# Optimization experiments

Hardware: AMD Instinct MI355X
Metric: run time of the kernel (lower is better)

The kernel has to match this reference:

```python
import jax, jax.numpy as jnp
import numpy as np

# Static config (matches init_kwargs)
DIM, HEADS = 192, 6
PL, LAT, LON = 8, 96, 180
WP, WL, WW = 2, 6, 12          # window size (pressure, lat, lon)
SP, SL, SW = 1, 3, 6           # shift size
N = WP * WL * WW               # tokens per window = 144
NPL, NLAT, NLON = PL // WP, LAT // WL, LON // WW   # 4, 16, 15
NW = NPL * NLAT                # type_of_windows = 64 (lat/pl-dependent bias)
HD = DIM // HEADS              # 32
L = PL * LAT * LON
BIAS_LEN = (2 * WW - 1) * WL * WL * WP * WP   # 3312
EPS = 1e-5


def _position_index():
    # Earth-specific relative position index (Pangu): absolute-position
    # dependence along pressure and latitude, relative along longitude.
    zi = np.arange(WP); zj = -np.arange(WP) * WP
    hi = np.arange(WL); hj = -np.arange(WL) * WL
    w = np.arange(WW)
    c1 = np.stack(np.meshgrid(zi, hi, w, indexing='ij')).reshape(3, -1)
    c2 = np.stack(np.meshgrid(zj, hj, w, indexing='ij')).reshape(3, -1)
    c = (c1[:, :, None] - c2[:, None, :]).transpose(1, 2, 0).copy()
    c[:, :, 2] += WW - 1
    c[:, :, 1] *= 2 * WW - 1
    c[:, :, 0] *= (2 * WW - 1) * WL * WL
    return c.sum(-1)  # (N, N) in [0, BIAS_LEN)


def _attn_mask():
    # Shifted-window mask: lon is periodic on the globe (roll only), so
    # masking is applied along pressure and latitude boundaries only.
    img = np.zeros((1, PL, LAT, LON, 1), np.float32)
    cnt = 0
    for pl in (slice(0, -WP), slice(-WP, -SP), slice(-SP, None)):
        for la in (slice(0, -WL), slice(-WL, -SL), slice(-SL, None)):
            img[:, pl, la, :, :] = cnt
            cnt += 1
    mw = img.reshape(1, NPL, WP, NLAT, WL, NLON, WW, 1)
    mw = mw.transpose(0, 5, 1, 3, 2, 4, 6, 7).reshape(NLON, NW, N)
    am = mw[:, :, None, :] - mw[:, :, :, None]
    return np.where(am != 0, -100.0, 0.0).astype(np.float32)  # (NLON, NW, N, N)


POS_IDX = jnp.asarray(_position_index())
ATTN_MASK = jnp.asarray(_attn_mask())


def layer_norm(x, g, b):
    m = x.mean(-1, keepdims=True)
    v = ((x - m) ** 2).mean(-1, keepdims=True)
    return (x - m) * jax.lax.rsqrt(v + EPS) * g + b


def setup_inputs() -> dict:
    key = jax.random.key(0)
    ks = jax.random.split(key, 10)
    s = 0.02
    return {
        'x': jax.random.normal(ks[0], (1, L, DIM), jnp.float32),
        'norm1_g': jnp.ones((DIM,), jnp.float32),
        'norm1_b': jnp.zeros((DIM,), jnp.float32),
        'qkv_w': jax.random.normal(ks[1], (DIM, 3 * DIM), jnp.float32) * s,
        'qkv_b': jnp.zeros((3 * DIM,), jnp.float32),
        'earth_bias': jax.random.normal(ks[2], (BIAS_LEN, NW, HEADS), jnp.float32) * s,
        'proj_w': jax.random.normal(ks[3], (DIM, DIM), jnp.float32) * s,
        'proj_b': jnp.zeros((DIM,), jnp.float32),
        'norm2_g': jnp.ones((DIM,), jnp.float32),
        'norm2_b': jnp.zeros((DIM,), jnp.float32),
        'fc1_w': jax.random.normal(ks[4], (DIM, 4 * DIM), jnp.float32) * s,
        'fc1_b': jnp.zeros((4 * DIM,), jnp.float32),
        'fc2_w': jax.random.normal(ks[5], (4 * DIM, DIM), jnp.float32) * s,
        'fc2_b': jnp.zeros((DIM,), jnp.float32),
    }


def reference(x, norm1_g, norm1_b, qkv_w, qkv_b, earth_bias, proj_w, proj_b,
              norm2_g, norm2_b, fc1_w, fc1_b, fc2_w, fc2_b):
    B, Ltok, C = x.shape
    shortcut = x
    h = layer_norm(x, norm1_g, norm1_b).reshape(B, PL, LAT, LON, C)
    # shifted windows (lon is periodic -> plain roll)
    h = jnp.roll(h, shift=(-SP, -SL, -SW), axis=(1, 2, 3))
    # window partition -> (B*NLON, NW, N, C); lon windows folded into batch
    xw = h.reshape(B, NPL, WP, NLAT, WL, NLON, WW, C)
    xw = xw.transpose(0, 5, 1, 3, 2, 4, 6, 7).reshape(B * NLON, NW, N, C)
    # earth-specific attention
    qkv = (xw @ qkv_w + qkv_b).reshape(B * NLON, NW, N, 3, HEADS, HD)
    qkv = qkv.transpose(3, 0, 1, 4, 2, 5)  # (3, B_, NW, H, N, HD)
    q, k, v = qkv[0], qkv[1], qkv[2]
    attn = jnp.einsum('bwhnd,bwhmd->bwhnm', q * (HD ** -0.5), k)
    bias = earth_bias[POS_IDX].reshape(N, N, NW, HEADS).transpose(2, 3, 0, 1)
    attn = attn + bias[None]                        # (B_, NW, H, N, N)
    attn = attn.reshape(B, NLON, NW, HEADS, N, N) + ATTN_MASK[None, :, :, None]
    attn = jax.nn.softmax(attn.reshape(B * NLON, NW, HEADS, N, N), axis=-1)
    out = jnp.einsum('bwhnm,bwhmd->bwhnd', attn, v)
    out = out.transpose(0, 1, 3, 2, 4).reshape(B * NLON, NW, N, C)
    out = out @ proj_w + proj_b
    # window reverse + roll back
    h = out.reshape(B, NLON, NPL, NLAT, WP, WL, WW, C)
    h = h.transpose(0, 2, 4, 3, 5, 1, 6, 7).reshape(B, PL, LAT, LON, C)
    h = jnp.roll(h, shift=(SP, SL, SW), axis=(1, 2, 3)).reshape(B, Ltok, C)
    x = shortcut + h
    # MLP block (GELU exact, as nn.GELU default)
    y = layer_norm(x, norm2_g, norm2_b)
    y = jax.nn.gelu(y @ fc1_w + fc1_b, approximate=False) @ fc2_w + fc2_b
    return x + y
```

## Files before the change

kernel.cpp:

```cpp
#include <hip/hip_runtime.h>
#include <hip/hip_bf16.h>
#include <math.h>

typedef unsigned short u16;
typedef __attribute__((ext_vector_type(8))) short short8;
typedef __attribute__((ext_vector_type(4))) short short4v;
typedef __attribute__((ext_vector_type(4))) float f32x4;

#define MFMA(a,b,c) __builtin_amdgcn_mfma_f32_16x16x32_bf16(a,b,c,0,0,0)
#define DIM 192

__device__ __forceinline__ float bf2f(u16 u){ unsigned v=((unsigned)u)<<16; float f; __builtin_memcpy(&f,&v,4); return f; }
__device__ __forceinline__ u16 f2bf(float f){ unsigned v; __builtin_memcpy(&v,&f,4); v = v + 0x7fffu + ((v>>16)&1u); return (u16)(v>>16); }

__device__ __forceinline__ void gl_lds16(const u16* g, u16* l){
  __builtin_amdgcn_global_load_lds((const __attribute__((address_space(1))) unsigned int*)g,
                                   (__attribute__((address_space(3))) unsigned int*)l, 16, 0, 0);
}

__device__ __forceinline__ int win_to_tok(int r){
  int lon = r/9216; int rem = r - lon*9216;
  int w = rem/144, n = rem - w*144;
  int ip=w>>4, il=w&15;
  int wp=n/72, t=n-wp*72, wl=t/12, ww=t-wl*12;
  int p=ip*2+wp, la=il*6+wl, lo=lon*12+ww;
  int p0=p+1;  if(p0>=8)   p0-=8;
  int la0=la+3; if(la0>=96) la0-=96;
  int lo0=lo+6; if(lo0>=180)lo0-=180;
  return (p0*96+la0)*180+lo0;
}

__global__ __launch_bounds__(256) void ln1_window_kernel(
    const float* __restrict__ x, const float* __restrict__ g, const float* __restrict__ b,
    u16* __restrict__ A)
{
  int r = blockIdx.x*4 + (threadIdx.x>>6);
  int lane = threadIdx.x & 63;
  size_t src = (size_t)win_to_tok(r)*DIM;
  float v0=x[src+lane], v1=x[src+64+lane], v2=x[src+128+lane];
  float s=v0+v1+v2;
  for(int m=32;m>=1;m>>=1) s += __shfl_xor(s,m);
  float mean = s*(1.f/192.f);
  float d0=v0-mean,d1=v1-mean,d2=v2-mean;
  float q=d0*d0+d1*d1+d2*d2;
  for(int m=32;m>=1;m>>=1) q += __shfl_xor(q,m);
  float rstd = rsqrtf(q*(1.f/192.f)+1e-5f);
  size_t o = (size_t)r*DIM;
  A[o+lane]     = f2bf(d0*rstd*g[lane]     + b[lane]);
  A[o+64+lane]  = f2bf(d1*rstd*g[64+lane]  + b[64+lane]);
  A[o+128+lane] = f2bf(d2*rstd*g[128+lane] + b[128+lane]);
}

__global__ __launch_bounds__(256) void transpose_bf16_kernel(
    const float* __restrict__ src, u16* __restrict__ dst, int K, int N)
{
  int idx = blockIdx.x*256 + threadIdx.x;
  if (idx >= K*N) return;
  int k = idx / N, n = idx - k*N;
  dst[n*K + k] = f2bf(src[idx]);
}

__global__ __launch_bounds__(256) void pf_w1_kernel(const float* __restrict__ fc1w, u16* __restrict__ W1f){
  int idx = blockIdx.x*256 + threadIdx.x;
  int e = idx & 7, g3 = idx >> 3;
  int g = g3 % 24, r3 = g3 / 24;
  int r = r3 & 31, hc = r3 >> 5;
  int k = ((g ^ (r&7))<<3) + e;
  W1f[idx] = f2bf(fc1w[(size_t)k*768 + hc*32 + r]);
}
__global__ __launch_bounds__(256) void pf_w2_kernel(const float* __restrict__ fc2w, u16* __restrict__ W2f){
  int idx = blockIdx.x*256 + threadIdx.x;
  int e = idx & 7, g3 = idx >> 3;
  int g = g3 & 3, r3 = g3 >> 2;
  int r = r3 % 192, hc = r3 / 192;
  int k = hc*32 + ((g ^ (r&3))<<3) + e;
  W2f[idx] = f2bf(fc2w[(size_t)k*192 + r]);
}

__global__ __launch_bounds__(256) void bias_expand_kernel(
    const float* __restrict__ eb, u16* __restrict__ B2)
{
  __shared__ int t1s[144], t2s[144], rgs[144];
  __shared__ float ebs[3312];
  int bid = blockIdx.x;
  int w = bid / 6;
  int tid = threadIdx.x;
  if (tid < 144) {
    int n = tid;
    int wp=n/72, t=n-wp*72, wl=t/12, ww=t-wl*12;
    t1s[n] = wp*828 + wl*23 + ww;
    t2s[n] = 1656*wp + 138*wl - ww + 11;
    int ip = w>>4, il = w&15;
    int p = ip*2+wp, la = il*6+wl;
    int rp = (p<6)?0:((p<7)?1:2);
    int rl = (la<90)?0:((la<93)?1:2);
    rgs[n] = rp*3+rl;
  }
  for (int i = tid; i < 3312; i += 256) ebs[i] = eb[(size_t)i*384 + bid];
  __syncthreads();
  size_t ob = (size_t)bid*20736;
  for (int idx = tid; idx < 20736; idx += 256) {
    int i = idx & 3, lane = (idx>>2)&63, t = idx>>8;
    int mt = t%9, nt = t/9;
    int n = nt*16 + (lane&15);
    int m = mt*16 + ((lane>>4)<<2) + i;
    float bv = ebs[t1s[n]+t2s[m]];
    bv += (rgs[n]==rgs[m]) ? 0.f : -100.f;
    B2[ob + idx] = f2bf(bv);
  }
}

#define SM_WS   0
#define SM_QS   36864
#define SM_KS   48384
#define SM_VS   59904
#define SM_PS   0
#define SMEM3   70656

__global__ __launch_bounds__(576) void attn_kernel(
    const u16* __restrict__ A,
    const u16* __restrict__ Wt,
    const float* __restrict__ qkvb,
    const u16* __restrict__ Bexp,
    u16* __restrict__ O)
{
  extern __shared__ char smem[];
  u16* Ws = (u16*)(smem + SM_WS);
  u16* qs = (u16*)(smem + SM_QS);
  u16* ks_= (u16*)(smem + SM_KS);
  u16* vs = (u16*)(smem + SM_VS);
  u16* Ps = (u16*)(smem + SM_PS);

  int bid = blockIdx.x;
  int logical = (bid & 7)*720 + (bid >> 3);
  int lon = logical % 15;
  int wh  = logical / 15;
  int h = wh % 6, w = wh / 6;
  int tid = threadIdx.x, lane = tid & 63, wv = tid >> 6;

  {
    int rr = tid % 96, chunk = tid / 96;
    int mat = rr >> 5, c = rr & 31;
    const u16* s = Wt + (size_t)(mat*192 + h*32 + c)*192 + chunk*32;
    uint4 t0 = *(const uint4*)(s);
    uint4 t1 = *(const uint4*)(s+8);
    uint4 t2 = *(const uint4*)(s+16);
    uint4 t3 = *(const uint4*)(s+24);
    u16* d = Ws + rr*192;
    int r7 = rr & 7, g0 = chunk*4;
    *(uint4*)(d + ((g0  )^r7)*8) = t0;
    *(uint4*)(d + ((g0+1)^r7)*8) = t1;
    *(uint4*)(d + ((g0+2)^r7)*8) = t2;
    *(uint4*)(d + ((g0+3)^r7)*8) = t3;
  }
  if (tid < 512) { int c = tid>>4; vs[c*168 + 144 + (tid&15)] = 0; }
  __syncthreads();

  size_t winbase = (size_t)(lon*64 + w)*144;
  int r0 = wv*16;
  int l15 = lane & 15, lg = lane >> 4;
  int sw7 = l15 & 7;

  short8 af[6];
  {
    const u16* arow = A + (winbase + r0 + l15)*DIM + 8*lg;
    #pragma unroll
    for (int k0=0;k0<6;k0++) af[k0] = *(const short8*)(arow + k0*32);
  }
  const float qscale = 0.17677669529663687f;

  #pragma unroll
  for (int mt=0; mt<2; mt++) {
    f32x4 acc = {0.f,0.f,0.f,0.f};
    const u16* wrow = Ws + (mt*16 + l15)*192;
    #pragma unroll
    for (int k0=0;k0<6;k0++) acc = MFMA(*(const short8*)(wrow + ((k0*4+lg)^sw7)*8), af[k0], acc);
    short4v pk;
    #pragma unroll
    for (int i=0;i<4;i++) pk[i] = (short)f2bf((acc[i] + qkvb[h*32 + mt*16 + 4*lg + i])*qscale);
    *(short4v*)(qs + (r0 + l15)*40 + mt*16 + 4*lg) = pk;
  }
  #pragma unroll
  for (int mt=0; mt<2; mt++) {
    f32x4 acc = {0.f,0.f,0.f,0.f};
    const u16* wrow = Ws + (32 + mt*16 + l15)*192;
    #pragma unroll
    for (int k0=0;k0<6;k0++) acc = MFMA(*(const short8*)(wrow + ((k0*4+lg)^sw7)*8), af[k0], acc);
    short4v pk;
    #pragma unroll
    for (int i=0;i<4;i++) pk[i] = (short)f2bf(acc[i] + qkvb[192 + h*32 + mt*16 + 4*lg + i]);
    *(short4v*)(ks_ + (r0 + l15)*40 + mt*16 + 4*lg) = pk;
  }
  #pragma unroll
  for (int ct=0; ct<2; ct++) {
    f32x4 acc = {0.f,0.f,0.f,0.f};
    const u16* wrow = Ws + (64 + ct*16 + l15)*192;
    #pragma unroll
    for (int k0=0;k0<6;k0++) acc = MFMA(af[k0], *(const short8*)(wrow + ((k0*4+lg)^sw7)*8), acc);
    float bias = qkvb[384 + h*32 + ct*16 + l15];
    short4v pk;
    #pragma unroll
    for (int i=0;i<4;i++) pk[i] = (short)f2bf(acc[i] + bias);
    *(short4v*)(vs + (ct*16 + l15)*168 + r0 + 4*lg) = pk;
  }
  __syncthreads();

  short8 bq = *(const short8*)(qs + (r0 + l15)*40 + 8*lg);
  f32x4 sa[9];
  #pragma unroll
  for (int mt=0; mt<9; mt++) {
    f32x4 z = {0.f,0.f,0.f,0.f};
    sa[mt] = MFMA(*(const short8*)(ks_ + (mt*16 + l15)*40 + 8*lg), bq, z);
  }
  __syncthreads();

  {
    const u16* bb = Bexp + (((size_t)wh*9 + wv)*9)*256 + lane*4;
    #pragma unroll
    for (int mt=0; mt<9; mt++) {
      short4v pk = *(const short4v*)(bb + mt*256);
      #pragma unroll
      for (int i=0;i<4;i++) sa[mt][i] += bf2f((u16)pk[i]);
    }
  }
  float rsum = 0.f;
  #pragma unroll
  for (int mt=0; mt<9; mt++)
    #pragma unroll
    for (int i=0;i<4;i++) { float e = __expf(sa[mt][i]); sa[mt][i] = e; rsum += e; }
  rsum += __shfl_xor(rsum, 16);
  rsum += __shfl_xor(rsum, 32);
  float rinv = 1.f / rsum;
  #pragma unroll
  for (int mt=0; mt<9; mt++) {
    short4v pk;
    #pragma unroll
    for (int i=0;i<4;i++) pk[i] = (short)f2bf(sa[mt][i]);
    *(short4v*)(Ps + (r0 + l15)*168 + mt*16 + 4*lg) = pk;
  }
  {
    short4v z = {0,0,0,0};
    *(short4v*)(Ps + (r0 + l15)*168 + 144 + 4*lg) = z;
  }

  #pragma unroll
  for (int ct2=0; ct2<2; ct2++) {
    f32x4 acc = {0.f,0.f,0.f,0.f};
    const u16* vr = vs + (ct2*16 + l15)*168 + 8*lg;
    const u16* pr = Ps + (r0 + l15)*168 + 8*lg;
    #pragma unroll
    for (int k0=0;k0<5;k0++) acc = MFMA(*(const short8*)(vr + 32*k0), *(const short8*)(pr + 32*k0), acc);
    short4v pk;
    #pragma unroll
    for (int i=0;i<4;i++) pk[i] = (short)f2bf(acc[i]*rinv);
    *(short4v*)(O + (winbase + r0 + l15)*DIM + h*32 + ct2*16 + 4*lg) = pk;
  }
}

#define SMEMF 74240
__global__ __launch_bounds__(512, 4) void fused_tail_kernel(
    u16* __restrict__ AT,
    const u16* __restrict__ Pw,
    const float* __restrict__ pb, const float* __restrict__ x,
    const float* __restrict__ n2g, const float* __restrict__ n2b,
    const u16* __restrict__ W1f,
    const float* __restrict__ b1,
    const u16* __restrict__ W2f,
    const float* __restrict__ b2,
    float* __restrict__ out)
{
  extern __shared__ char smem[];
  u16* Pws  = (u16*)smem;
  u16* Ys   = (u16*)smem;
  u16* W1b0 = (u16*)smem;
  u16* W1b1 = (u16*)(smem + 12288);
  u16* W2b0 = (u16*)(smem + 24576);
  u16* W2b1 = (u16*)(smem + 36864);
  u16* Hs   = (u16*)(smem + 49152);
  int* tokmap = (int*)(smem + 73728);
  int tid = threadIdx.x;
  size_t rbase = (size_t)blockIdx.x*128;
  int lane = tid&63, wv = tid>>6, r0 = wv*16;
  int l15 = lane&15, lg = lane>>4;

  #pragma unroll
  for (int j=0;j<9;j++){
    int g = j*512 + tid;
    int row = g/24, jj = g - row*24;
    uint4 t = *(const uint4*)(Pw + (size_t)row*192 + jj*8);
    *(uint4*)(Pws + row*192 + ((jj ^ (row&7))*8)) = t;
  }
  if (tid < 128) tokmap[tid] = win_to_tok((int)rbase + tid);
  __syncthreads();

  short8 af[6];
  {
    const u16* arow = AT + (rbase + r0 + l15)*DIM + 8*lg;
    #pragma unroll
    for (int k0=0;k0<6;k0++) af[k0] = *(const short8*)(arow + k0*32);
  }
  f32x4 acc[12];
  #pragma unroll
  for (int ct=0; ct<12; ct++) {
    f32x4 a = {0.f,0.f,0.f,0.f};
    const u16* wr = Pws + (ct*16+l15)*192;
    #pragma unroll
    for (int k0=0;k0<6;k0++) a = MFMA(af[k0], *(const short8*)(wr + (((k0*4+lg)^(l15&7))*8)), a);
    acc[ct] = a;
  }
  int toks[4];
  #pragma unroll
  for (int i=0;i<4;i++) toks[i] = tokmap[r0 + 4*lg + i];

  #pragma unroll
  for (int ct=0; ct<12; ct++) {
    int col = ct*16+l15;
    float bias = pb[col];
    #pragma unroll
    for (int i=0;i<4;i++){
      float v = x[(size_t)toks[i]*DIM + col] + acc[ct][i] + bias;
      acc[ct][i] = v;
      AT[(rbase + r0 + 4*lg + i)*DIM + col] = f2bf(v);
    }
  }
  float s[4] = {0,0,0,0};
  #pragma unroll
  for (int ct=0; ct<12; ct++) for (int i=0;i<4;i++) s[i] += acc[ct][i];
  #pragma unroll
  for (int i=0;i<4;i++){ for (int m=1;m<16;m<<=1) s[i] += __shfl_xor(s[i], m, 16); s[i] *= (1.f/192.f); }
  float q[4] = {0,0,0,0};
  #pragma unroll
  for (int ct=0; ct<12; ct++) for (int i=0;i<4;i++){ float d = acc[ct][i]-s[i]; q[i] += d*d; }
  #pragma unroll
  for (int i=0;i<4;i++){ for (int m=1;m<16;m<<=1) q[i] += __shfl_xor(q[i], m, 16); q[i] = rsqrtf(q[i]*(1.f/192.f)+1e-5f); }

  __syncthreads();
  #pragma unroll
  for (int ct=0; ct<12; ct++) {
    int col = ct*16+l15;
    float gg = n2g[col], bb = n2b[col];
    #pragma unroll
    for (int i=0;i<4;i++)
      Ys[(r0 + 4*lg + i)*200 + col] = f2bf((acc[ct][i]-s[i])*q[i]*gg + bb);
  }
  #pragma unroll
  for (int k0=0;k0<6;k0++) af[k0] = *(const short8*)(Ys + (r0+l15)*200 + k0*32 + 8*lg);
  __syncthreads();

  {
    gl_lds16(W1f + (size_t)tid*8, W1b0 + tid*8);
    if (tid < 256) gl_lds16(W1f + (size_t)(512+tid)*8, W1b0 + (512+tid)*8);
    gl_lds16(W2f + (size_t)tid*8, W2b0 + tid*8);
    if (tid < 256) gl_lds16(W2f + (size_t)(512+tid)*8, W2b0 + (512+tid)*8);
    const u16* s1 = W1f + 6144; const u16* s2 = W2f + 6144;
    gl_lds16(s1 + (size_t)tid*8, W1b1 + tid*8);
    if (tid < 256) gl_lds16(s1 + (size_t)(512+tid)*8, W1b1 + (512+tid)*8);
    gl_lds16(s2 + (size_t)tid*8, W2b1 + tid*8);
    if (tid < 256) gl_lds16(s2 + (size_t)(512+tid)*8, W2b1 + (512+tid)*8);
  }
  __syncthreads();

  f32x4 acc2[12];
  #pragma unroll
  for (int i=0;i<12;i++) acc2[i] = (f32x4){0.f,0.f,0.f,0.f};

  const float GA = -1.5957691216057307f;
  const float GB = -0.07135481627272283f;

  for (int hc=0; hc<24; hc++) {
    u16* B1w = (hc&1) ? W1b1 : W1b0;
    u16* B2w = (hc&1) ? W2b1 : W2b0;
    #pragma unroll
    for (int ct=0; ct<2; ct++) {
      f32x4 a1 = {0.f,0.f,0.f,0.f};
      const u16* wr = B1w + (ct*16+l15)*192;
      #pragma unroll
      for (int k0=0;k0<6;k0++) a1 = MFMA(af[k0], *(const short8*)(wr + (((k0*4+lg)^(l15&7))*8)), a1);
      float bb = b1[hc*32 + ct*16 + l15];
      #pragma unroll
      for (int i=0;i<4;i++){
        float v = a1[i] + bb;
        float t = v*v;
        float m = fmaf(t, GB, GA);
        float e = __expf(v*m);
        float hgl = v*__builtin_amdgcn_rcpf(1.f + e);
        Hs[(r0 + 4*lg + i)*40 + ct*16 + l15] = f2bf(hgl);
      }
    }
    {
      short8 ah = *(const short8*)(Hs + (r0+l15)*40 + 8*lg);
      #pragma unroll
      for (int ct2=0; ct2<12; ct2++) {
        const u16* wr2 = B2w + (ct2*16+l15)*32 + ((lg ^ (l15&3))*8);
        acc2[ct2] = MFMA(ah, *(const short8*)(wr2), acc2[ct2]);
      }
    }
    __syncthreads();
    if (hc < 22) {
      const u16* s1 = W1f + (size_t)(hc+2)*6144;
      const u16* s2 = W2f + (size_t)(hc+2)*6144;
      u16* d1 = (hc&1) ? W1b1 : W1b0;
      u16* d2 = (hc&1) ? W2b1 : W2b0;
      gl_lds16(s1 + (size_t)tid*8, d1 + tid*8);
      if (tid < 256) gl_lds16(s1 + (size_t)(512+tid)*8, d1 + (512+tid)*8);
      gl_lds16(s2 + (size_t)tid*8, d2 + tid*8);
      if (tid < 256) gl_lds16(s2 + (size_t)(512+tid)*8, d2 + (512+tid)*8);
    }
  }
  #pragma unroll
  for (int ct2=0; ct2<12; ct2++) {
    int col = ct2*16+l15;
    float bb = b2[col];
    #pragma unroll
    for (int i=0;i<4;i++){
      float x2v = bf2f(AT[(rbase + r0 + 4*lg + i)*DIM + col]);
      out[(size_t)toks[i]*DIM + col] = x2v + acc2[ct2][i] + bb;
    }
  }
}

extern "C" void kernel_launch(void* const* d_in, const int* in_sizes, int n_in,
                              void* d_out, int out_size, void* d_ws, size_t ws_size,
                              hipStream_t stream) {
  const float* x    = (const float*)d_in[0];
  const float* n1g  = (const float*)d_in[1];
  const float* n1b  = (const float*)d_in[2];
  const float* qkvw = (const float*)d_in[3];
  const float* qkvb = (const float*)d_in[4];
  const float* eb   = (const float*)d_in[5];
  const float* projw= (const float*)d_in[6];
  const float* projb= (const float*)d_in[7];
  const float* n2g  = (const float*)d_in[8];
  const float* n2b  = (const float*)d_in[9];
  const float* fc1w = (const float*)d_in[10];
  const float* fc1b = (const float*)d_in[11];
  const float* fc2w = (const float*)d_in[12];
  const float* fc2b = (const float*)d_in[13];
  float* out = (float*)d_out;
  char* ws = (char*)d_ws;

  u16* A   = (u16*)(ws);
  u16* AT  = (u16*)(ws + 53084160);
  u16* Wq  = (u16*)(ws + 106168320);
  u16* Pw  = (u16*)(ws + 106389504);
  u16* W1f = (u16*)(ws + 106463232);
  u16* W2f = (u16*)(ws + 106758144);
  u16* Bexp = (u16*)d_out;

  hipFuncSetAttribute((const void*)attn_kernel,       hipFuncAttributeMaxDynamicSharedMemorySize, SMEM3);
  hipFuncSetAttribute((const void*)fused_tail_kernel, hipFuncAttributeMaxDynamicSharedMemorySize, SMEMF);

  transpose_bf16_kernel<<<432, 256, 0, stream>>>(qkvw, Wq, 192, 576);
  transpose_bf16_kernel<<<144, 256, 0, stream>>>(projw, Pw, 192, 192);
  pf_w1_kernel<<<576, 256, 0, stream>>>(fc1w, W1f);
  pf_w2_kernel<<<576, 256, 0, stream>>>(fc2w, W2f);
  bias_expand_kernel<<<384, 256, 0, stream>>>(eb, Bexp);
  ln1_window_kernel<<<34560, 256, 0, stream>>>(x, n1g, n1b, A);
  attn_kernel<<<5760, 576, SMEM3, stream>>>(A, Wq, qkvb, Bexp, AT);
  fused_tail_kernel<<<1080, 512, SMEMF, stream>>>(AT, Pw, projb, x, n2g, n2b,
                                                  W1f, fc1b, W2f, fc2b, out);
}
```

Before: 421.7 us.

## Software-pipeline FC1/GELU of next chunk with FC2 of current chunk

Restructures the MLP hidden-chunk loop in the fused tail kernel into a software pipeline. The FC1 GEMM and GELU for chunk hc+1 now run in the same iteration as the FC2 GEMM for chunk hc, using a double-buffered hidden tile (HsA/HsB) in LDS. The aim is to give each wave independent MFMA and transcendental work to interleave, instead of a serial FC1, then GELU, then FC2 chain. W2 weights are now prefetched one chunk ahead rather than two, and their loads are issued at the start of the iteration. That leaves less time to hide global-to-LDS latency for W2, and the extra live state raises register pressure.

After: 406.3 us. -3.7%, faster.

```diff
diff --git a/kernel.cpp b/kernel.cpp
--- a/kernel.cpp
+++ b/kernel.cpp
@@ -276,7 +276,8 @@
   u16* W1b1 = (u16*)(smem + 12288);
   u16* W2b0 = (u16*)(smem + 24576);
   u16* W2b1 = (u16*)(smem + 36864);
-  u16* Hs   = (u16*)(smem + 49152);
+  u16* HsA  = (u16*)(smem + 49152);
+  u16* HsB  = (u16*)(smem + 59392);
   int* tokmap = (int*)(smem + 73728);
   int tid = threadIdx.x;
   size_t rbase = (size_t)blockIdx.x*128;
@@ -352,11 +353,9 @@
     if (tid < 256) gl_lds16(W1f + (size_t)(512+tid)*8, W1b0 + (512+tid)*8);
     gl_lds16(W2f + (size_t)tid*8, W2b0 + tid*8);
     if (tid < 256) gl_lds16(W2f + (size_t)(512+tid)*8, W2b0 + (512+tid)*8);
-    const u16* s1 = W1f + 6144; const u16* s2 = W2f + 6144;
+    const u16* s1 = W1f + 6144;
     gl_lds16(s1 + (size_t)tid*8, W1b1 + tid*8);
     if (tid < 256) gl_lds16(s1 + (size_t)(512+tid)*8, W1b1 + (512+tid)*8);
-    gl_lds16(s2 + (size_t)tid*8, W2b1 + tid*8);
-    if (tid < 256) gl_lds16(s2 + (size_t)(512+tid)*8, W2b1 + (512+tid)*8);
   }
   __syncthreads();
 
@@ -367,45 +366,68 @@
   const float GA = -1.5957691216057307f;
   const float GB = -0.07135481627272283f;
 
+  #pragma unroll
+  for (int ct=0; ct<2; ct++) {
+    f32x4 a1 = {0.f,0.f,0.f,0.f};
+    const u16* wr = W1b0 + (ct*16+l15)*192;
+    #pragma unroll
+    for (int k0=0;k0<6;k0++) a1 = MFMA(af[k0], *(const short8*)(wr + (((k0*4+lg)^(l15&7))*8)), a1);
+    float bb = b1[ct*16 + l15];
+    #pragma unroll
+    for (int i=0;i<4;i++){
+      float v = a1[i] + bb;
+      float t = v*v;
+      float m = fmaf(t, GB, GA);
+      float e = __expf(v*m);
+      HsA[(r0 + 4*lg + i)*40 + ct*16 + l15] = f2bf(v*__builtin_amdgcn_rcpf(1.f + e));
+    }
+  }
+  __syncthreads();
+
   for (int hc=0; hc<24; hc++) {
-    u16* B1w = (hc&1) ? W1b1 : W1b0;
-    u16* B2w = (hc&1) ? W2b1 : W2b0;
-    #pragma unroll
-    for (int ct=0; ct<2; ct++) {
-      f32x4 a1 = {0.f,0.f,0.f,0.f};
-      const u16* wr = B1w + (ct*16+l15)*192;
-      #pragma unroll
-      for (int k0=0;k0<6;k0++) a1 = MFMA(af[k0], *(const short8*)(wr + (((k0*4+lg)^(l15&7))*8)), a1);
-      float bb = b1[hc*32 + ct*16 + l15];
-      #pragma unroll
-      for (int i=0;i<4;i++){
-        float v = a1[i] + bb;
-        float t = v*v;
-        float m = fmaf(t, GB, GA);
-        float e = __expf(v*m);
-        float hgl = v*__builtin_amdgcn_rcpf(1.f + e);
-        Hs[(r0 + 4*lg + i)*40 + ct*16 + l15] = f2bf(hgl);
-      }
+    u16* HsCur = (hc&1) ? HsB : HsA;
+    u16* HsNxt = (hc&1) ? HsA : HsB;
+    u16* W2cur = (hc&1) ? W2b1 : W2b0;
+    u16* W1nxt = (hc&1) ? W1b0 : W1b1;
+    if (hc+2 < 24) {
+      const u16* s1 = W1f + (size_t)(hc+2)*6144;
+      u16* d1 = (hc&1) ? W1b1 : W1b0;
+      gl_lds16(s1 + (size_t)tid*8, d1 + tid*8);
+      if (tid < 256) gl_lds16(s1 + (size_t)(512+tid)*8, d1 + (512+tid)*8);
+    }
+    if (hc+1 < 24) {
+      const u16* s2 = W2f + (size_t)(hc+1)*6144;
+      u16* d2 = (hc&1) ? W2b0 : W2b1;
+      gl_lds16(s2 + (size_t)tid*8, d2 + tid*8);
+      if (tid < 256) gl_lds16(s2 + (size_t)(512+tid)*8, d2 + (512+tid)*8);
     }
     {
-      short8 ah = *(const short8*)(Hs + (r0+l15)*40 + 8*lg);
+      short8 ah = *(const short8*)(HsCur + (r0+l15)*40 + 8*lg);
       #pragma unroll
       for (int ct2=0; ct2<12; ct2++) {
-        const u16* wr2 = B2w + (ct2*16+l15)*32 + ((lg ^ (l15&3))*8);
+        const u16* wr2 = W2cur + (ct2*16+l15)*32 + ((lg ^ (l15&3))*8);
         acc2[ct2] = MFMA(ah, *(const short8*)(wr2), acc2[ct2]);
       }
     }
+    if (hc+1 < 24) {
+      #pragma unroll
+      for (int ct=0; ct<2; ct++) {
+        f32x4 a1 = {0.f,0.f,0.f,0.f};
+        const u16* wr = W1nxt + (ct*16+l15)*192;
+        #pragma unroll
+        for (int k0=0;k0<6;k0++) a1 = MFMA(af[k0], *(const short8*)(wr + (((k0*4+lg)^(l15&7))*8)), a1);
+        float bb = b1[(hc+1)*32 + ct*16 + l15];
+        #pragma unroll
+        for (int i=0;i<4;i++){
+          float v = a1[i] + bb;
+          float t = v*v;
+          float m = fmaf(t, GB, GA);
+          float e = __expf(v*m);
+          HsNxt[(r0 + 4*lg + i)*40 + ct*16 + l15] = f2bf(v*__builtin_amdgcn_rcpf(1.f + e));
+        }
+      }
+    }
     __syncthreads();
-    if (hc < 22) {
-      const u16* s1 = W1f + (size_t)(hc+2)*6144;
-      const u16* s2 = W2f + (size_t)(hc+2)*6144;
-      u16* d1 = (hc&1) ? W1b1 : W1b0;
-      u16* d2 = (hc&1) ? W2b1 : W2b0;
-      gl_lds16(s1 + (size_t)tid*8, d1 + tid*8);
-      if (tid < 256) gl_lds16(s1 + (size_t)(512+tid)*8, d1 + (512+tid)*8);
-      gl_lds16(s2 + (size_t)tid*8, d2 + tid*8);
-      if (tid < 256) gl_lds16(s2 + (size_t)(512+tid)*8, d2 + (512+tid)*8);
-    }
   }
   #pragma unroll
   for (int ct2=0; ct2<12; ct2++) {
```
